# Performance work log

Hardware: AMD Instinct MI355X
Metric: run time of the kernel (lower is better)

## Reference

```python
import jax, jax.numpy as jnp
import numpy as np

N_ELEC, N_ATOMS, FEAT = 2048, 512, 128
N_UP = 1024  # spins = (1024, 1024)
NUM_RBF = 32
DIM = 256
TANH_GAIN = 5.0 / 3.0  # ActivationWithGain assumed: activation(x) * gain (tanh gain)


def setup_inputs() -> dict:
    key = jax.random.key(0)
    k1, k2, k3 = jax.random.split(key, 3)
    h_one_two = jax.random.normal(k1, (N_ELEC, N_ATOMS, FEAT), dtype=jnp.float32)
    r_im_norm = jax.random.uniform(k2, (N_ELEC, N_ATOMS), dtype=jnp.float32) * 10.0
    # GaussRBF params
    mu = jnp.linspace(0, NUM_RBF - 1, NUM_RBF, dtype=jnp.float32)[None, None, :]  # (1,1,K)
    sigma = jnp.ones((1, 1, NUM_RBF), dtype=jnp.float32) * 10.0
    # Dense(dim) on concat of spin means: in = 2*FEAT
    W = jax.random.normal(k3, (2 * FEAT, DIM), dtype=jnp.float32) / np.sqrt(2 * FEAT)
    b = jnp.zeros((DIM,), dtype=jnp.float32)
    return {"h_one_two": h_one_two, "r_im_norm": r_im_norm, "mu": mu, "sigma": sigma, "W": W, "b": b}


def reference(h_one_two, r_im_norm, mu, sigma, W, b):
    # GaussRBF: (E,A,1) vs (1,1,K) -> (E,A,K), mean over K -> (E,A,1)
    d = r_im_norm[..., None] - mu
    rbf = jnp.exp(-(d * d) / jax.nn.softplus(sigma)).mean(-1, keepdims=True)
    h = h_one_two * rbf  # (E,A,F)
    # spin-split mean pooling over electrons
    up = h[:N_UP].mean(0, keepdims=True)   # (1,A,F)
    dn = h[N_UP:].mean(0, keepdims=True)   # (1,A,F)
    atom_emb = jnp.concatenate([up, dn], axis=-1)  # (1,A,2F)
    atom_emb = jnp.tanh(atom_emb @ W + b) * TANH_GAIN  # (1,A,DIM)
    elec_emb = h.mean(1, keepdims=True)  # (E,1,F)
    return atom_emb, elec_emb
```

## Files before the change

### kernel.cpp

```cpp
#include <hip/hip_runtime.h>
#include <cstdint>
#include <cstddef>

#define E_TOT 2048
#define A_TOT 512
#define FEAT  128
#define N_UP  1024
#define K_RBF 32
#define DIM   256

typedef float vfloat4 __attribute__((ext_vector_type(4)));

template <int EB>
__global__ __launch_bounds__(256) void main_pass(
    const float* __restrict__ h, const float* __restrict__ r_im,
    const float* __restrict__ mu, const float* __restrict__ sigma,
    float* __restrict__ ws_atom,
    float* __restrict__ ws_elec) {
  constexpr int AB = 128;
  constexpr int GA = A_TOT / AB;
  const int bid = blockIdx.x;
  const int g_a = bid % GA, g_e = bid / GA;
  const int e0 = g_e * EB, a0 = g_a * AB;
  const int t = threadIdx.x;
  const int wave = t >> 6, lane = t & 63;
  const int f4 = lane & 31, r_lo = lane >> 5;

  __shared__ float s_mu[K_RBF], s_inv[K_RBF];
  __shared__ float rbf_lds[EB * AB];
  __shared__ float esum_lds[EB * FEAT];

  if (t < K_RBF) {
    s_mu[t] = mu[t];
    float s = sigma[t];
    float sp = (s > 20.0f) ? s : log1pf(__expf(s));
    s_inv[t] = 1.0f / sp;
  }
  __syncthreads();

  for (int i = t; i < EB * FEAT; i += 256) esum_lds[i] = 0.0f;
  for (int i = t; i < EB * AB; i += 256) {
    int e_l = i / AB, a_l = i % AB;
    float rv = r_im[(size_t)(e0 + e_l) * A_TOT + a0 + a_l];
    float acc = 0.0f;
#pragma unroll
    for (int k = 0; k < K_RBF; ++k) {
      float d = rv - s_mu[k];
      acc += __expf(-d * d * s_inv[k]);
    }
    rbf_lds[i] = acc * (1.0f / K_RBF);
  }
  __syncthreads();

  vfloat4 acc[16];
#pragma unroll
  for (int i = 0; i < 16; ++i) acc[i] = (vfloat4)(0.f);

  const float* hbase = h + ((size_t)e0 * A_TOT + a0) * FEAT +
                       (wave * 32 + r_lo) * FEAT + f4 * 4;
  const int arb = wave * 32 + r_lo;

  auto ldchunk = [&](vfloat4* buf, int e, int c) {
#pragma unroll
    for (int i = 0; i < 8; ++i) {
      const float* p = hbase + (size_t)e * (A_TOT * FEAT) +
                       (c * 8 + i) * (2 * FEAT);
      buf[i] = __builtin_nontemporal_load(reinterpret_cast<const vfloat4*>(p));
    }
  };

  vfloat4 esum;
  auto prchunk = [&](vfloat4* buf, int e, int c) {
#pragma unroll
    for (int i = 0; i < 8; ++i) {
      const int j = c * 8 + i;
      float rb = rbf_lds[e * AB + arb + j * 2];
      vfloat4 v = buf[i] * rb;
      acc[j] += v;
      esum += v;
    }
  };

  vfloat4 B0[8], B1[8];
  ldchunk(B0, 0, 0);
  ldchunk(B1, 0, 1);
  for (int e = 0; e < EB; ++e) {
    esum = (vfloat4)(0.f);
    prchunk(B0, e, 0);
    if (e + 1 < EB) ldchunk(B0, e + 1, 0);
    prchunk(B1, e, 1);
    if (e + 1 < EB) ldchunk(B1, e + 1, 1);
    esum.x += __shfl_down(esum.x, 32, 64);
    esum.y += __shfl_down(esum.y, 32, 64);
    esum.z += __shfl_down(esum.z, 32, 64);
    esum.w += __shfl_down(esum.w, 32, 64);
    if (lane < 32) {
      float* p = &esum_lds[e * FEAT + f4 * 4];
      atomicAdd(p + 0, esum.x);
      atomicAdd(p + 1, esum.y);
      atomicAdd(p + 2, esum.z);
      atomicAdd(p + 3, esum.w);
    }
  }

  vfloat4* ws_a4 = reinterpret_cast<vfloat4*>(ws_atom);
#pragma unroll
  for (int j = 0; j < 16; ++j) {
    const int a_l = wave * 32 + j * 2 + r_lo;
    ws_a4[((size_t)g_e * A_TOT + a0 + a_l) * 32 + f4] = acc[j];
  }

  __syncthreads();
  vfloat4* ws_e4 = reinterpret_cast<vfloat4*>(ws_elec);
  const vfloat4* es4 = reinterpret_cast<const vfloat4*>(esum_lds);
  for (int i = t; i < EB * 32; i += 256) {
    const int e_l = i >> 5, ff = i & 31;
    ws_e4[((size_t)g_a * E_TOT + e0 + e_l) * 32 + ff] = es4[e_l * 32 + ff];
  }
}

__global__ __launch_bounds__(256) void finals(
    const float* __restrict__ ws_atom, const float* __restrict__ ws_elec,
    const float* __restrict__ W, const float* __restrict__ bias,
    float* __restrict__ out, int ge_total, int slices) {
  const int t = threadIdx.x;
  if (blockIdx.x < A_TOT) {
    const int a = blockIdx.x;
    __shared__ float s_in[2 * FEAT];
    const int spin = t >> 7;
    const int f = t & 127;
    const int gh = ge_total >> 1;
    const int g0 = spin * gh;
    float acc = 0.0f;
#pragma unroll 4
    for (int g = 0; g < gh; ++g) {
      acc += ws_atom[((size_t)(g0 + g) * A_TOT + a) * FEAT + f];
    }
    s_in[t] = acc * (1.0f / (float)N_UP);
    __syncthreads();
    float o = bias[t];
#pragma unroll 4
    for (int k = 0; k < 2 * FEAT; ++k) {
      o += s_in[k] * W[(size_t)k * DIM + t];
    }
    out[(size_t)a * DIM + t] = tanhf(o) * (5.0f / 3.0f);
  } else {
    const int idx = (int)(blockIdx.x - A_TOT) * 256 + t;
    const int n4 = E_TOT * FEAT / 4;
    const vfloat4* in4 = reinterpret_cast<const vfloat4*>(ws_elec);
    vfloat4 s = (vfloat4)(0.f);
    for (int g = 0; g < slices; ++g) {
      s += in4[(size_t)g * n4 + idx];
    }
    s *= (1.0f / (float)A_TOT);
    reinterpret_cast<vfloat4*>(out + (size_t)A_TOT * DIM)[idx] = s;
  }
}

extern "C" void kernel_launch(void* const* d_in, const int* in_sizes, int n_in,
                              void* d_out, int out_size, void* d_ws, size_t ws_size,
                              hipStream_t stream) {
  const float* h     = (const float*)d_in[0];
  const float* r_im  = (const float*)d_in[1];
  const float* mu    = (const float*)d_in[2];
  const float* sigma = (const float*)d_in[3];
  const float* W     = (const float*)d_in[4];
  const float* b     = (const float*)d_in[5];
  float* out = (float*)d_out;

  float* ws_atom = (float*)d_ws;
  const int finals_grid = A_TOT + (E_TOT * FEAT / 4) / 256;
  constexpr int GA = 4;

  const size_t need16 = ((size_t)(E_TOT / 16) * A_TOT * FEAT +
                         (size_t)GA * E_TOT * FEAT) * 4;
  if (ws_size >= need16) {
    constexpr int GE = E_TOT / 16;
    float* ws_elec = ws_atom + (size_t)GE * A_TOT * FEAT;
    main_pass<16><<<GE * GA, 256, 0, stream>>>(h, r_im, mu, sigma, ws_atom, ws_elec);
    finals<<<finals_grid, 256, 0, stream>>>(ws_atom, ws_elec, W, b, out, GE, GA);
  } else {
    constexpr int GE = E_TOT / 32;
    float* ws_elec = ws_atom + (size_t)GE * A_TOT * FEAT;
    main_pass<32><<<GE * GA, 256, 0, stream>>>(h, r_im, mu, sigma, ws_atom, ws_elec);
    finals<<<finals_grid, 256, 0, stream>>>(ws_atom, ws_elec, W, b, out, GE, GA);
  }
}
```

Measured before the change: 129.3 us.

## Double-buffer whole electron rows, add occupancy hint, transpose atom workspace layout

The main loop now prefetches one full electron row of 16 vectors into a second register buffer while the current row is processed, replacing the half-row chunked prefetch. This deepens the number of loads in flight. A launch-bounds minimum of 2 blocks per SM is added, and the partial-atom workspace is re-laid out atom-major so that the finals kernel reads each atom's partials contiguously. The extra register buffer raises register pressure, which could cause spills under the occupancy constraint.

```diff
diff --git a/kernel.cpp b/kernel.cpp
--- a/kernel.cpp
+++ b/kernel.cpp
@@ -12,13 +12,14 @@
 typedef float vfloat4 __attribute__((ext_vector_type(4)));
 
 template <int EB>
-__global__ __launch_bounds__(256) void main_pass(
+__global__ __launch_bounds__(256, 2) void main_pass(
     const float* __restrict__ h, const float* __restrict__ r_im,
     const float* __restrict__ mu, const float* __restrict__ sigma,
     float* __restrict__ ws_atom,
     float* __restrict__ ws_elec) {
   constexpr int AB = 128;
   constexpr int GA = A_TOT / AB;
+  constexpr int GE = E_TOT / EB;
   const int bid = blockIdx.x;
   const int g_a = bid % GA, g_e = bid / GA;
   const int e0 = g_e * EB, a0 = g_a * AB;
@@ -60,36 +61,22 @@
                        (wave * 32 + r_lo) * FEAT + f4 * 4;
   const int arb = wave * 32 + r_lo;
 
-  auto ldchunk = [&](vfloat4* buf, int e, int c) {
+  auto ldall = [&](vfloat4* buf, int e) {
 #pragma unroll
-    for (int i = 0; i < 8; ++i) {
-      const float* p = hbase + (size_t)e * (A_TOT * FEAT) +
-                       (c * 8 + i) * (2 * FEAT);
+    for (int i = 0; i < 16; ++i) {
+      const float* p = hbase + (size_t)e * (A_TOT * FEAT) + i * (2 * FEAT);
       buf[i] = __builtin_nontemporal_load(reinterpret_cast<const vfloat4*>(p));
     }
   };
-
-  vfloat4 esum;
-  auto prchunk = [&](vfloat4* buf, int e, int c) {
+  auto prall = [&](const vfloat4* buf, int e) {
+    vfloat4 esum = (vfloat4)(0.f);
 #pragma unroll
-    for (int i = 0; i < 8; ++i) {
-      const int j = c * 8 + i;
-      float rb = rbf_lds[e * AB + arb + j * 2];
+    for (int i = 0; i < 16; ++i) {
+      float rb = rbf_lds[e * AB + arb + i * 2];
       vfloat4 v = buf[i] * rb;
-      acc[j] += v;
+      acc[i] += v;
       esum += v;
     }
-  };
-
-  vfloat4 B0[8], B1[8];
-  ldchunk(B0, 0, 0);
-  ldchunk(B1, 0, 1);
-  for (int e = 0; e < EB; ++e) {
-    esum = (vfloat4)(0.f);
-    prchunk(B0, e, 0);
-    if (e + 1 < EB) ldchunk(B0, e + 1, 0);
-    prchunk(B1, e, 1);
-    if (e + 1 < EB) ldchunk(B1, e + 1, 1);
     esum.x += __shfl_down(esum.x, 32, 64);
     esum.y += __shfl_down(esum.y, 32, 64);
     esum.z += __shfl_down(esum.z, 32, 64);
@@ -101,13 +88,23 @@
       atomicAdd(p + 2, esum.z);
       atomicAdd(p + 3, esum.w);
     }
+  };
+
+  vfloat4 B[16], C[16];
+  static_assert(EB % 2 == 0, "EB even");
+  ldall(B, 0);
+  for (int e = 0; e < EB; e += 2) {
+    if (e + 1 < EB) ldall(C, e + 1);
+    prall(B, e);
+    if (e + 2 < EB) ldall(B, e + 2);
+    prall(C, e + 1);
   }
 
   vfloat4* ws_a4 = reinterpret_cast<vfloat4*>(ws_atom);
 #pragma unroll
   for (int j = 0; j < 16; ++j) {
     const int a_l = wave * 32 + j * 2 + r_lo;
-    ws_a4[((size_t)g_e * A_TOT + a0 + a_l) * 32 + f4] = acc[j];
+    ws_a4[((size_t)(a0 + a_l) * GE + g_e) * 32 + f4] = acc[j];
   }
 
   __syncthreads();
@@ -131,10 +128,11 @@
     const int f = t & 127;
     const int gh = ge_total >> 1;
     const int g0 = spin * gh;
+    const float* base = ws_atom + ((size_t)a * ge_total + g0) * FEAT + f;
     float acc = 0.0f;
 #pragma unroll 4
     for (int g = 0; g < gh; ++g) {
-      acc += ws_atom[((size_t)(g0 + g) * A_TOT + a) * FEAT + f];
+      acc += base[(size_t)g * FEAT];
     }
     s_in[t] = acc * (1.0f / (float)N_UP);
     __syncthreads();
```

After: 224.3 us. 73.4% more time.
